# Kernel optimization log

Hardware: AMD Instinct MI355X
Metric: run time of the kernel (lower is better)

## Reference

```python
import jax, jax.numpy as jnp
import numpy as np

KS = 3
PAD = 1
STRIDE = 1


def _conv2d(x, w, b=None, stride=1, padding=0):
    out = jax.lax.conv_general_dilated(
        x, w, (stride, stride), [(padding, padding), (padding, padding)],
        dimension_numbers=("NCHW", "OIHW", "NCHW"))
    if b is not None:
        out = out + b[None, :, None, None]
    return out


def _p_n(N):
    # torch.meshgrid(a, a, indexing='xy') -> X[i,j]=a[j], Y[i,j]=a[i]
    a = np.arange(-(KS - 1) // 2, (KS - 1) // 2 + 1)
    X, Y = np.meshgrid(a, a, indexing="xy")
    p_n = np.concatenate([X.flatten(), Y.flatten()], 0).astype(np.float32)
    return jnp.asarray(p_n.reshape(1, 2 * N, 1, 1))


def _p_0(h, w, N):
    av = np.arange(1, h * STRIDE + 1, STRIDE)
    bv = np.arange(1, w * STRIDE + 1, STRIDE)
    X, Y = np.meshgrid(av, bv, indexing="xy")  # shape (w, h), replicates torch quirk
    p0x = np.tile(X.flatten().reshape(1, 1, h, w), (1, N, 1, 1))
    p0y = np.tile(Y.flatten().reshape(1, 1, h, w), (1, N, 1, 1))
    return jnp.asarray(np.concatenate([p0x, p0y], 1).astype(np.float32))


def setup_inputs() -> dict:
    key = jax.random.key(0)
    k1, k2, k3, k4 = jax.random.split(key, 4)
    B, C, H, W = 2, 64, 256, 256
    x = jax.random.normal(k1, (B, C, H, W), dtype=jnp.float32)
    p_conv_w = jax.random.normal(k2, (2 * KS * KS, C, 3, 3), dtype=jnp.float32) * 0.01
    p_conv_b = jax.random.normal(k3, (2 * KS * KS,), dtype=jnp.float32) * 0.1
    conv_w = jax.random.normal(k4, (64, C, KS, KS), dtype=jnp.float32) * 0.05
    return {"x": x, "p_conv_w": p_conv_w, "p_conv_b": p_conv_b, "conv_w": conv_w}


def _deform_conv(x, p_conv_w, p_conv_b, conv_w):
    B, C = x.shape[0], x.shape[1]
    offset = _conv2d(x, p_conv_w, p_conv_b, stride=STRIDE, padding=1)  # (B, 2N, h, w)
    N = offset.shape[1] // 2
    h, w = offset.shape[2], offset.shape[3]
    xp = jnp.pad(x, ((0, 0), (0, 0), (PAD, PAD), (PAD, PAD)))
    Hp, Wp = xp.shape[2], xp.shape[3]

    p = _p_0(h, w, N) + _p_n(N) + offset            # (B, 2N, h, w)
    p = p.transpose(0, 2, 3, 1)                      # (B, h, w, 2N)

    def clampxy(t):
        return jnp.concatenate(
            [jnp.clip(t[..., :N], 0, Hp - 1), jnp.clip(t[..., N:], 0, Wp - 1)], -1)

    q_lt = clampxy(jnp.floor(jax.lax.stop_gradient(p)))
    q_rb = clampxy(jnp.floor(jax.lax.stop_gradient(p)) + 1)
    q_lt = q_lt.astype(jnp.int32)
    q_rb = q_rb.astype(jnp.int32)
    q_lb = jnp.concatenate([q_lt[..., :N], q_rb[..., N:]], -1)
    q_rt = jnp.concatenate([q_rb[..., :N], q_lt[..., N:]], -1)

    p = clampxy(p)
    px, py = p[..., :N], p[..., N:]

    def bilin_w(q):
        qx = q[..., :N].astype(p.dtype)
        qy = q[..., N:].astype(p.dtype)
        return qx - px, qy - py

    dx_lt, dy_lt = bilin_w(q_lt)
    dx_rb, dy_rb = bilin_w(q_rb)
    g_lt = (1 + dx_lt) * (1 + dy_lt)
    g_rb = (1 - dx_rb) * (1 - dy_rb)
    g_lb = (1 + dx_lt) * (1 - dy_rb)   # q_lb = (lt_x, rb_y)
    g_rt = (1 - dx_rb) * (1 + dy_lt)   # q_rt = (rb_x, lt_y)

    xf = xp.reshape(B, C, Hp * Wp)

    def gather(q):
        idx = q[..., :N] * Wp + q[..., N:]                     # (B, h, w, N)
        idxb = jnp.broadcast_to(idx.reshape(B, 1, -1), (B, C, h * w * N))
        return jnp.take_along_axis(xf, idxb, axis=2).reshape(B, C, h, w, N)

    x_off = (g_lt[:, None] * gather(q_lt) + g_rb[:, None] * gather(q_rb)
             + g_lb[:, None] * gather(q_lb) + g_rt[:, None] * gather(q_rt))

    # 'b c h w (kh kw) -> b c (h kh) (w kw)'
    x_off = x_off.reshape(B, C, h, w, KS, KS).transpose(0, 1, 2, 4, 3, 5)
    x_off = x_off.reshape(B, C, h * KS, w * KS)
    return _conv2d(x_off, conv_w, stride=KS)


def reference(x, p_conv_w, p_conv_b, conv_w):
    return _deform_conv(x, p_conv_w, p_conv_b, conv_w)
```

## Files before the change

### kernel.cpp

```cpp
#include <hip/hip_runtime.h>

#define HW   256
#define HW2  (HW * HW)
#define CIN  64
#define COUT 64

#define RXN   7
#define CYN   70
#define NSITE (RXN * CYN)
#define SSTR  48

#define ONS   198
#define OSTR  144

typedef __attribute__((ext_vector_type(8))) short short8v;
typedef __attribute__((ext_vector_type(4))) float f32x4;
typedef __attribute__((ext_vector_type(4))) unsigned uint4v;

__device__ __forceinline__ unsigned short f2bf(float f) {
  unsigned u = __float_as_uint(f);
  u = u + 0x7FFFu + ((u >> 16) & 1u);
  return (unsigned short)(u >> 16);
}
__device__ __forceinline__ unsigned cvt_pk_bf16(float lo, float hi) {
  unsigned r;
  asm("v_cvt_pk_bf16_f32 %0, %1, %2" : "=v"(r) : "v"(lo), "v"(hi));
  return r;
}

__global__ void wfrag_kernel(const float* __restrict__ w, const float* __restrict__ pw,
                             short* __restrict__ wf, short* __restrict__ wf2) {
  const int T = blockIdx.x * 256 + threadIdx.x;
  if (T < 5120) {
    const int l    = T & 63;
    const int t    = (T >> 6) & 3;
    const int g    = T >> 8;
    const int j    = g % 5;
    const int rho  = g / 5;
    const int half = (l >> 5) & 1;
    const int oct  = (l >> 4) & 1;
    const int n    = 2 * j + half;
    const int oc   = t * 16 + (l & 15);
    const int ic0  = rho * 16 + oct * 8;
    short8v v;
#pragma unroll
    for (int e = 0; e < 8; ++e)
      v[e] = (n < 9) ? (short)f2bf(w[(oc * CIN + ic0 + e) * 9 + n]) : (short)0;
    *(short8v*)(wf + (size_t)T * 8) = v;
  } else if (T < 7680) {
    const int T2   = T - 5120;
    const int l    = T2 & 63;
    const int t    = (T2 >> 6) & 1;
    const int g    = T2 >> 7;
    const int j    = g % 5;
    const int rho  = g / 5;
    const int half = (l >> 5) & 1;
    const int oct  = (l >> 4) & 1;
    const int n    = 2 * j + half;
    const int oc   = t * 16 + (l & 15);
    const int ic0  = rho * 16 + oct * 8;
    short8v v;
#pragma unroll
    for (int e = 0; e < 8; ++e)
      v[e] = (n < 9 && oc < 18) ? (short)f2bf(pw[(oc * CIN + ic0 + e) * 9 + n])
                                : (short)0;
    *(short8v*)(wf2 + (size_t)T2 * 8) = v;
  }
}

__global__ __launch_bounds__(256) void offs_mfma_kernel(
    const float* __restrict__ x, const short* __restrict__ wf2,
    const float* __restrict__ pb, float* __restrict__ off)
{
  __shared__ __align__(16) char sow[ONS * OSTR];

  const int b    = blockIdx.y;
  const int bx   = blockIdx.x;
  const int r0   = (bx & 3) * 64;
  const int c0   = bx >> 2;
  const int tid  = threadIdx.x;
  const int lane = tid & 63;
  const int i    = lane & 15;
  const int g4   = lane >> 4;
  const int oct  = g4 & 1;
  const int half = g4 >> 1;
  const int wv   = tid >> 6;
  const int r    = r0 + wv * 16 + i;

  if (tid < ONS) {
    const int rl = tid / 3, kw = tid - rl * 3;
    const int rr = r0 - 1 + rl;
    const int cc = c0 - 1 + kw;
    const bool ok = (rr >= 0) & (rr < HW) & (cc >= 0) & (cc < HW);
    const float* xq = x + (size_t)b * CIN * HW2
                    + (size_t)max(rr, 0) * HW + max(cc, 0);
    char* dst = sow + tid * OSTR;
#pragma unroll
    for (int m8 = 0; m8 < 8; ++m8) {
      uint4v v;
#pragma unroll
      for (int mm = 0; mm < 4; ++mm) {
        const int pl = m8 * 8 + mm * 2;
        const float v0 = ok ? xq[(size_t)pl * HW2] : 0.f;
        const float v1 = ok ? xq[(size_t)(pl + 1) * HW2] : 0.f;
        v[mm] = cvt_pk_bf16(v0, v1);
      }
      *(uint4v*)(dst + m8 * 16) = v;
    }
  }
  __syncthreads();

  f32x4 acc0 = (f32x4){0.f, 0.f, 0.f, 0.f};
  f32x4 acc1 = (f32x4){0.f, 0.f, 0.f, 0.f};

#pragma unroll
  for (int rho = 0; rho < 4; ++rho) {
#pragma unroll
    for (int j = 0; j < 5; ++j) {
      const int n  = 2 * j + half;
      const int nn = (n < 9) ? n : 0;
      const int kh = nn / 3, kw = nn - kh * 3;
      const int site = (wv * 16 + i + kh) * 3 + kw;
      const short8v bfr = *(const short8v*)(sow + site * OSTR + rho * 32 + oct * 16);
      const short* wfb = wf2 + ((size_t)(((rho * 5 + j) * 2) * 64) + lane) * 8;
      const short8v a0 = *(const short8v*)(wfb);
      const short8v a1 = *(const short8v*)(wfb + 64 * 8);
      acc0 = __builtin_amdgcn_mfma_f32_16x16x32_bf16(a0, bfr, acc0, 0, 0, 0);
      acc1 = __builtin_amdgcn_mfma_f32_16x16x32_bf16(a1, bfr, acc1, 0, 0, 0);
    }
  }

  float* ob = off + (size_t)(b * HW + c0) * 18 * HW;
#pragma unroll
  for (int jj = 0; jj < 4; ++jj) {
    const int ch = g4 * 4 + jj;
    ob[(size_t)ch * HW + r] = acc0[jj] + pb[ch];
  }
  if (g4 == 0) {
#pragma unroll
    for (int jj = 0; jj < 2; ++jj) {
      const int ch = 16 + jj;
      ob[(size_t)ch * HW + r] = acc1[jj] + pb[ch];
    }
  }
}

__global__ __launch_bounds__(256)
__attribute__((amdgpu_waves_per_eu(2, 4)))
void deform_kernel(
    const float* __restrict__ x, const float* __restrict__ off,
    const short* __restrict__ wf, float* __restrict__ out)
{
  __shared__ __align__(16) char sxb[NSITE * SSTR];

  const int b    = blockIdx.y;
  const int bx   = blockIdx.x;
  const int r0   = (bx & 3) * 64;
  const int c0   = bx >> 2;
  const int tid  = threadIdx.x;
  const int lane = tid & 63;
  const int i    = lane & 15;
  const int a    = (lane >> 4) & 3;
  const int oct  = a & 1;
  const int half = a >> 1;
  const int wv   = tid >> 6;
  const int r    = r0 + wv * 16 + i;

  unsigned qsite[5];
  float    qwx[5], qwy[5];
  unsigned inwm = 0;
  const float* obp = off + (size_t)(b * HW + c0) * 18 * HW;
#pragma unroll
  for (int t5 = 0; t5 < 5; ++t5) {
    const int  n9  = 2 * t5 + half;
    const bool pad = (n9 >= 9);
    const int  n   = pad ? 0 : n9;
    const float ox = obp[(size_t)n * HW + r];
    const float oy = obp[(size_t)(9 + n) * HW + r];
    const float px = (float)(c0 + (n % 3)) + ox;
    const float py = (float)(r + (n / 3)) + oy;
    const float fx = floorf(px);
    const float fy = floorf(py);
    const int ltx = (int)fx, lty = (int)fy;
    const bool okc = (ltx >= 0) & (lty >= 0) & (ltx + 1 <= HW + 1) & (lty + 1 <= HW + 1);
    const int lx = ltx - c0 + 2;
    const int ly = lty - r0 + 2;
    const bool inw = okc & (lx >= 0) & (lx <= RXN - 2) & (ly >= 0) & (ly <= CYN - 2);
    qsite[t5] = (pad || !inw) ? 0u : (unsigned)(lx * CYN + ly);
    qwx[t5]   = 1.f + fx - px;
    qwy[t5]   = 1.f + fy - py;
    inwm |= ((inw || pad) ? 1u : 0u) << t5;
  }

  const int s1 = tid, s2 = tid + 256;
  int gi1 = 0, gi2 = 0; bool ok1, ok2;
  {
    const int rxl = s1 / CYN, cyl = s1 - rxl * CYN;
    const int rx = c0 - 2 + rxl, cyp = r0 - 2 + cyl;
    ok1 = (rx >= 1) & (rx <= HW) & (cyp >= 1) & (cyp <= HW);
    if (ok1) gi1 = (rx - 1) * HW + (cyp - 1);
  }
  {
    const int rxl = s2 / CYN, cyl = s2 - rxl * CYN;
    const int rx = c0 - 2 + rxl, cyp = r0 - 2 + cyl;
    ok2 = (s2 < NSITE) & (rx >= 1) & (rx <= HW) & (cyp >= 1) & (cyp <= HW);
    if (ok2) gi2 = (rx - 1) * HW + (cyp - 1);
  }

  const float* xb = x + (size_t)b * CIN * HW2;

  float pv1[16], pv2[16];

#define LOADR(RHO)                                                         \
  {                                                                        \
    const float* xsrc = xb + (size_t)((RHO) * 16) * HW2;                   \
    _Pragma("unroll")                                                      \
    for (int m = 0; m < 16; ++m) {                                         \
      const float* xp = xsrc + (size_t)m * HW2;                            \
      pv1[m] = ok1 ? xp[gi1] : 0.f;                                        \
      pv2[m] = ok2 ? xp[gi2] : 0.f;                                        \
    }                                                                      \
  }

#define WRITES()                                                           \
  {                                                                        \
    uint4v w0, w1;                                                         \
    _Pragma("unroll")                                                      \
    for (int m = 0; m < 4; ++m) w0[m] = cvt_pk_bf16(pv1[2*m], pv1[2*m+1]); \
    _Pragma("unroll")                                                      \
    for (int m = 0; m < 4; ++m) w1[m] = cvt_pk_bf16(pv1[8+2*m], pv1[9+2*m]);\
    *(uint4v*)(sxb + s1 * SSTR)      = w0;                                 \
    *(uint4v*)(sxb + s1 * SSTR + 16) = w1;                                 \
    if (s2 < NSITE) {                                                      \
      uint4v u0, u1;                                                       \
      _Pragma("unroll")                                                    \
      for (int m = 0; m < 4; ++m) u0[m] = cvt_pk_bf16(pv2[2*m], pv2[2*m+1]);\
      _Pragma("unroll")                                                    \
      for (int m = 0; m < 4; ++m) u1[m] = cvt_pk_bf16(pv2[8+2*m], pv2[9+2*m]);\
      *(uint4v*)(sxb + s2 * SSTR)      = u0;                               \
      *(uint4v*)(sxb + s2 * SSTR + 16) = u1;                               \
    }                                                                      \
  }

  f32x4 acc[4];
#pragma unroll
  for (int t = 0; t < 4; ++t) acc[t] = (f32x4){0.f, 0.f, 0.f, 0.f};

  LOADR(0)
  WRITES()
  __syncthreads();

#pragma unroll 1
  for (int rho = 0; rho < 4; ++rho) {
    if (rho < 3) LOADR(rho + 1)

    const short* wfr = wf + ((size_t)(rho * 5 * 4) * 64 + lane) * 8;
    const char*  sbo = sxb + oct * 16;

    uint4v nA, nB, nC, nD;
    {
      const char* pb_ = sbo + qsite[0] * SSTR;
      nA = *(const uint4v*)(pb_);
      nC = *(const uint4v*)(pb_ + SSTR);
      nD = *(const uint4v*)(pb_ + 70 * SSTR);
      nB = *(const uint4v*)(pb_ + 71 * SSTR);
    }

#define TAPBODY(J)                                                          \
    {                                                                       \
       \
      const short* wfb_ = wfr + (size_t)(J) * 4 * 64 * 8;                   \
      const short8v af0 = *(const short8v*)(wfb_);                          \
      const short8v af1 = *(const short8v*)(wfb_ + 1 * 64 * 8);             \
      const short8v af2 = *(const short8v*)(wfb_ + 2 * 64 * 8);             \
      const short8v af3 = *(const short8v*)(wfb_ + 3 * 64 * 8);             \
      const uint4v A = nA, B = nB, C = nC, D = nD;                          \
      if ((J) < 4) {                       \
        const char* pb_ = sbo + qsite[(J) + 1] * SSTR;                      \
        nA = *(const uint4v*)(pb_);                                         \
        nC = *(const uint4v*)(pb_ + SSTR);                                  \
        nD = *(const uint4v*)(pb_ + 70 * SSTR);                             \
        nB = *(const uint4v*)(pb_ + 71 * SSTR);                             \
      }                                                                     \
      short8v bfr;                                                          \
      if (__all((inwm >> (J)) & 1)) {                                       \
        const float wxl = qwx[J], wyl = qwy[J];                             \
        const float wxr = 1.f - wxl, wyr = 1.f - wyl;                       \
        const float g0 = wxl * wyl, g1 = wxr * wyr;                         \
        const float g2 = wxl * wyr, g3 = wxr * wyl;                         \
        uint4v bw;                                                          \
        _Pragma("unroll")                                                   \
        for (int m = 0; m < 4; ++m) {                                       \
          const float alo = __uint_as_float(A[m] << 16);                    \
          const float ahi = __uint_as_float(A[m] & 0xFFFF0000u);            \
          const float blo = __uint_as_float(B[m] << 16);                    \
          const float bhi = __uint_as_float(B[m] & 0xFFFF0000u);            \
          const float clo = __uint_as_float(C[m] << 16);                    \
          const float chi = __uint_as_float(C[m] & 0xFFFF0000u);            \
          const float dlo = __uint_as_float(D[m] << 16);                    \
          const float dhi = __uint_as_float(D[m] & 0xFFFF0000u);            \
          float sl = g0 * alo;                                              \
          sl = fmaf(g1, blo, sl); sl = fmaf(g2, clo, sl);                   \
          sl = fmaf(g3, dlo, sl);                                           \
          float sh = g0 * ahi;                                              \
          sh = fmaf(g1, bhi, sh); sh = fmaf(g2, chi, sh);                   \
          sh = fmaf(g3, dhi, sh);                                           \
          bw[m] = cvt_pk_bf16(sl, sh);                                      \
        }                                                                   \
        bfr = __builtin_bit_cast(short8v, bw);                              \
      } else {                                                              \
         \
        const int  n9_  = 2 * (J) + half;                                   \
        const bool pad_ = (n9_ >= 9);                                       \
        const int  n_   = pad_ ? 0 : n9_;                                   \
        const float ox_ = obp[(size_t)n_ * HW + r];                         \
        const float oy_ = obp[(size_t)(9 + n_) * HW + r];                   \
        const float px_ = (float)(c0 + (n_ % 3)) + ox_;                     \
        const float py_ = (float)(r + (n_ / 3)) + oy_;                      \
        const float fx_ = floorf(px_);                                      \
        const float fy_ = floorf(py_);                                      \
        int ltx_ = (int)fx_, lty_ = (int)fy_;                               \
        int rbx_ = ltx_ + 1, rby_ = lty_ + 1;                               \
        ltx_ = min(max(ltx_, 0), HW + 1); lty_ = min(max(lty_, 0), HW + 1); \
        rbx_ = min(max(rbx_, 0), HW + 1); rby_ = min(max(rby_, 0), HW + 1); \
        const float pxc_ = fminf(fmaxf(px_, 0.f), (float)(HW + 1));         \
        const float pyc_ = fminf(fmaxf(py_, 0.f), (float)(HW + 1));         \
        const float wxl_ = 1.f + (float)ltx_ - pxc_;                        \
        const float wxr_ = 1.f - ((float)rbx_ - pxc_);                      \
        const float wyl_ = 1.f + (float)lty_ - pyc_;                        \
        const float wyr_ = 1.f - ((float)rby_ - pyc_);                      \
        const int   cxs_[4] = { ltx_, rbx_, ltx_, rbx_ };                   \
        const int   cys_[4] = { lty_, rby_, rby_, lty_ };                   \
        const float cgs_[4] = { wxl_ * wyl_, wxr_ * wyr_,                   \
                                wxl_ * wyr_, wxr_ * wyl_ };                 \
        int gi_[4]; float gw_[4];                                           \
        _Pragma("unroll")                                                   \
        for (int k = 0; k < 4; ++k) {                                       \
          const bool ok_ = (cxs_[k] >= 1) & (cxs_[k] <= HW) &               \
                           (cys_[k] >= 1) & (cys_[k] <= HW);                \
          gi_[k] = ok_ ? ((cxs_[k] - 1) * HW + (cys_[k] - 1)) : 0;          \
          gw_[k] = (ok_ && !pad_) ? cgs_[k] : 0.f;                          \
        }                                                                   \
        const float* xpl_ = xb + (size_t)(rho * 16 + oct * 8) * HW2;        \
        _Pragma("unroll")                                                   \
        for (int e = 0; e < 8; ++e) {                                       \
          const float* xe_ = xpl_ + (size_t)e * HW2;                        \
          float sv_ = gw_[0] * xe_[gi_[0]];                                 \
          sv_ = fmaf(gw_[1], xe_[gi_[1]], sv_);                             \
          sv_ = fmaf(gw_[2], xe_[gi_[2]], sv_);                             \
          sv_ = fmaf(gw_[3], xe_[gi_[3]], sv_);                             \
          bfr[e] = (short)f2bf(sv_);                                        \
        }                                                                   \
      }                                                                     \
      acc[0] = __builtin_amdgcn_mfma_f32_16x16x32_bf16(af0, bfr, acc[0], 0, 0, 0); \
      acc[1] = __builtin_amdgcn_mfma_f32_16x16x32_bf16(af1, bfr, acc[1], 0, 0, 0); \
      acc[2] = __builtin_amdgcn_mfma_f32_16x16x32_bf16(af2, bfr, acc[2], 0, 0, 0); \
      acc[3] = __builtin_amdgcn_mfma_f32_16x16x32_bf16(af3, bfr, acc[3], 0, 0, 0); \
    }

    TAPBODY(0) TAPBODY(1) TAPBODY(2) TAPBODY(3) TAPBODY(4)
#undef TAPBODY

    __syncthreads();
    if (rho < 3) {
      WRITES()
      __syncthreads();
    }
  }

#pragma unroll
  for (int t = 0; t < 4; ++t)
#pragma unroll
    for (int jj = 0; jj < 4; ++jj) {
      const int oc = t * 16 + a * 4 + jj;
      out[((size_t)(b * COUT + oc)) * HW2 + (size_t)r * HW + c0] = acc[t][jj];
    }
#undef LOADR
#undef WRITES
}

extern "C" void kernel_launch(void* const* d_in, const int* in_sizes, int n_in,
                              void* d_out, int out_size, void* d_ws, size_t ws_size,
                              hipStream_t stream) {
  const float* x  = (const float*)d_in[0];
  const float* pw = (const float*)d_in[1];
  const float* pb = (const float*)d_in[2];
  const float* w  = (const float*)d_in[3];
  float* out = (float*)d_out;

  char* wsb = (char*)d_ws;
  float* off = (float*)wsb;
  short* wfg = (short*)(wsb + (size_t)2 * 18 * HW2 * 4);
  short* wf2 = (short*)(wsb + (size_t)2 * 18 * HW2 * 4 + 81920);

  wfrag_kernel<<<30, 256, 0, stream>>>(w, pw, wfg, wf2);
  dim3 grid(1024, 2);
  offs_mfma_kernel<<<grid, 256, 0, stream>>>(x, wf2, pb, off);
  deform_kernel<<<grid, 256, 0, stream>>>(x, off, wfg, out);
}
```

Measured before the change: 164.3 us.

## Fuse offset-conv MFMA kernel into deform kernel via shared-memory offsets

Merges the offset convolution kernel into the deformable sampling kernel. Each block first computes its 18 offset channels for its 64-pixel column tile with MFMA and stores them in LDS, then runs the deform gather and conv reading offsets from LDS instead of a global buffer. This removes the global round-trip of the offset tensor and one kernel launch. In exchange LDS use per block grows, which may reduce occupancy, and the offset stage's x staging is serialized ahead of the deform work in the same block.

```diff
diff --git a/kernel.cpp b/kernel.cpp
--- a/kernel.cpp
+++ b/kernel.cpp
@@ -13,8 +13,10 @@
 #define ONS   198
 #define OSTR  144
 
-typedef __attribute__((ext_vector_type(8))) short short8v;
-typedef __attribute__((ext_vector_type(4))) float f32x4;
+#define SOFF_BYTES 4608
+
+typedef __attribute__((ext_vector_type(8))) short    short8v;
+typedef __attribute__((ext_vector_type(4))) float    f32x4;
 typedef __attribute__((ext_vector_type(4))) unsigned uint4v;
 
 __device__ __forceinline__ unsigned short f2bf(float f) {
@@ -68,90 +70,17 @@
   }
 }
 
-__global__ __launch_bounds__(256) void offs_mfma_kernel(
-    const float* __restrict__ x, const short* __restrict__ wf2,
-    const float* __restrict__ pb, float* __restrict__ off)
-{
-  __shared__ __align__(16) char sow[ONS * OSTR];
-
-  const int b    = blockIdx.y;
-  const int bx   = blockIdx.x;
-  const int r0   = (bx & 3) * 64;
-  const int c0   = bx >> 2;
-  const int tid  = threadIdx.x;
-  const int lane = tid & 63;
-  const int i    = lane & 15;
-  const int g4   = lane >> 4;
-  const int oct  = g4 & 1;
-  const int half = g4 >> 1;
-  const int wv   = tid >> 6;
-  const int r    = r0 + wv * 16 + i;
-
-  if (tid < ONS) {
-    const int rl = tid / 3, kw = tid - rl * 3;
-    const int rr = r0 - 1 + rl;
-    const int cc = c0 - 1 + kw;
-    const bool ok = (rr >= 0) & (rr < HW) & (cc >= 0) & (cc < HW);
-    const float* xq = x + (size_t)b * CIN * HW2
-                    + (size_t)max(rr, 0) * HW + max(cc, 0);
-    char* dst = sow + tid * OSTR;
-#pragma unroll
-    for (int m8 = 0; m8 < 8; ++m8) {
-      uint4v v;
-#pragma unroll
-      for (int mm = 0; mm < 4; ++mm) {
-        const int pl = m8 * 8 + mm * 2;
-        const float v0 = ok ? xq[(size_t)pl * HW2] : 0.f;
-        const float v1 = ok ? xq[(size_t)(pl + 1) * HW2] : 0.f;
-        v[mm] = cvt_pk_bf16(v0, v1);
-      }
-      *(uint4v*)(dst + m8 * 16) = v;
-    }
-  }
-  __syncthreads();
-
-  f32x4 acc0 = (f32x4){0.f, 0.f, 0.f, 0.f};
-  f32x4 acc1 = (f32x4){0.f, 0.f, 0.f, 0.f};
-
-#pragma unroll
-  for (int rho = 0; rho < 4; ++rho) {
-#pragma unroll
-    for (int j = 0; j < 5; ++j) {
-      const int n  = 2 * j + half;
-      const int nn = (n < 9) ? n : 0;
-      const int kh = nn / 3, kw = nn - kh * 3;
-      const int site = (wv * 16 + i + kh) * 3 + kw;
-      const short8v bfr = *(const short8v*)(sow + site * OSTR + rho * 32 + oct * 16);
-      const short* wfb = wf2 + ((size_t)(((rho * 5 + j) * 2) * 64) + lane) * 8;
-      const short8v a0 = *(const short8v*)(wfb);
-      const short8v a1 = *(const short8v*)(wfb + 64 * 8);
-      acc0 = __builtin_amdgcn_mfma_f32_16x16x32_bf16(a0, bfr, acc0, 0, 0, 0);
-      acc1 = __builtin_amdgcn_mfma_f32_16x16x32_bf16(a1, bfr, acc1, 0, 0, 0);
-    }
-  }
-
-  float* ob = off + (size_t)(b * HW + c0) * 18 * HW;
-#pragma unroll
-  for (int jj = 0; jj < 4; ++jj) {
-    const int ch = g4 * 4 + jj;
-    ob[(size_t)ch * HW + r] = acc0[jj] + pb[ch];
-  }
-  if (g4 == 0) {
-#pragma unroll
-    for (int jj = 0; jj < 2; ++jj) {
-      const int ch = 16 + jj;
-      ob[(size_t)ch * HW + r] = acc1[jj] + pb[ch];
-    }
-  }
-}
-
 __global__ __launch_bounds__(256)
 __attribute__((amdgpu_waves_per_eu(2, 4)))
-void deform_kernel(
-    const float* __restrict__ x, const float* __restrict__ off,
-    const short* __restrict__ wf, float* __restrict__ out)
+void fused_kernel(
+    const float* __restrict__ x, const short* __restrict__ wf,
+    const short* __restrict__ wf2, const float* __restrict__ pb,
+    float* __restrict__ out)
 {
-  __shared__ __align__(16) char sxb[NSITE * SSTR];
+  __shared__ __align__(16) char smem[SOFF_BYTES + ONS * OSTR];
+  float* sOffT = (float*)smem;
+  char*  sow   = smem + SOFF_BYTES;
+  char*  sxb   = smem + SOFF_BYTES;
 
   const int b    = blockIdx.y;
   const int bx   = blockIdx.x;
@@ -164,19 +93,77 @@
   const int oct  = a & 1;
   const int half = a >> 1;
   const int wv   = tid >> 6;
-  const int r    = r0 + wv * 16 + i;
+  const int rr   = wv * 16 + i;
+  const int r    = r0 + rr;
+
+  const float* xb = x + (size_t)b * CIN * HW2;
+
+  if (tid < ONS) {
+    const int rl = tid / 3, kw = tid - rl * 3;
+    const int rw = r0 - 1 + rl;
+    const int cc = c0 - 1 + kw;
+    const bool ok = (rw >= 0) & (rw < HW) & (cc >= 0) & (cc < HW);
+    const float* xq = xb + (size_t)max(rw, 0) * HW + max(cc, 0);
+    char* dst = sow + tid * OSTR;
+#pragma unroll
+    for (int m8 = 0; m8 < 8; ++m8) {
+      uint4v v;
+#pragma unroll
+      for (int mm = 0; mm < 4; ++mm) {
+        const int pl = m8 * 8 + mm * 2;
+        const float v0 = ok ? xq[(size_t)pl * HW2] : 0.f;
+        const float v1 = ok ? xq[(size_t)(pl + 1) * HW2] : 0.f;
+        v[mm] = cvt_pk_bf16(v0, v1);
+      }
+      *(uint4v*)(dst + m8 * 16) = v;
+    }
+  }
+  __syncthreads();
+
+  {
+    f32x4 acc0 = (f32x4){0.f, 0.f, 0.f, 0.f};
+    f32x4 acc1 = (f32x4){0.f, 0.f, 0.f, 0.f};
+#pragma unroll
+    for (int rho = 0; rho < 4; ++rho) {
+#pragma unroll
+      for (int j = 0; j < 5; ++j) {
+        const int n  = 2 * j + half;
+        const int nn = (n < 9) ? n : 0;
+        const int kh = nn / 3, kw = nn - kh * 3;
+        const int site = (rr + kh) * 3 + kw;
+        const short8v bfr = *(const short8v*)(sow + site * OSTR + rho * 32 + oct * 16);
+        const short* wfb = wf2 + ((size_t)(((rho * 5 + j) * 2) * 64) + lane) * 8;
+        const short8v a0 = *(const short8v*)(wfb);
+        const short8v a1 = *(const short8v*)(wfb + 64 * 8);
+        acc0 = __builtin_amdgcn_mfma_f32_16x16x32_bf16(a0, bfr, acc0, 0, 0, 0);
+        acc1 = __builtin_amdgcn_mfma_f32_16x16x32_bf16(a1, bfr, acc1, 0, 0, 0);
+      }
+    }
+#pragma unroll
+    for (int jj = 0; jj < 4; ++jj) {
+      const int ch = a * 4 + jj;
+      sOffT[ch * 64 + rr] = acc0[jj] + pb[ch];
+    }
+    if (a == 0) {
+#pragma unroll
+      for (int jj = 0; jj < 2; ++jj) {
+        const int ch = 16 + jj;
+        sOffT[ch * 64 + rr] = acc1[jj] + pb[ch];
+      }
+    }
+  }
+  __syncthreads();
 
   unsigned qsite[5];
   float    qwx[5], qwy[5];
   unsigned inwm = 0;
-  const float* obp = off + (size_t)(b * HW + c0) * 18 * HW;
 #pragma unroll
   for (int t5 = 0; t5 < 5; ++t5) {
     const int  n9  = 2 * t5 + half;
     const bool pad = (n9 >= 9);
     const int  n   = pad ? 0 : n9;
-    const float ox = obp[(size_t)n * HW + r];
-    const float oy = obp[(size_t)(9 + n) * HW + r];
+    const float ox = sOffT[n * 64 + rr];
+    const float oy = sOffT[(9 + n) * 64 + rr];
     const float px = (float)(c0 + (n % 3)) + ox;
     const float py = (float)(r + (n / 3)) + oy;
     const float fx = floorf(px);
@@ -206,8 +193,6 @@
     ok2 = (s2 < NSITE) & (rx >= 1) & (rx <= HW) & (cyp >= 1) & (cyp <= HW);
     if (ok2) gi2 = (rx - 1) * HW + (cyp - 1);
   }
-
-  const float* xb = x + (size_t)b * CIN * HW2;
 
   float pv1[16], pv2[16];
 
@@ -275,8 +260,8 @@
       const short8v af2 = *(const short8v*)(wfb_ + 2 * 64 * 8);             \
       const short8v af3 = *(const short8v*)(wfb_ + 3 * 64 * 8);             \
       const uint4v A = nA, B = nB, C = nC, D = nD;                          \
-      if ((J) < 4) {                       \
-        const char* pb_ = sbo + qsite[(J) + 1] * SSTR;                      \
+      if ((J) < 4) {               \
+        const char* pb_ = sbo + qsite[(J) < 4 ? (J) + 1 : 0] * SSTR;        \
         nA = *(const uint4v*)(pb_);                                         \
         nC = *(const uint4v*)(pb_ + SSTR);                                  \
         nD = *(const uint4v*)(pb_ + 70 * SSTR);                             \
@@ -313,8 +298,8 @@
         const int  n9_  = 2 * (J) + half;                                   \
         const bool pad_ = (n9_ >= 9);                                       \
         const int  n_   = pad_ ? 0 : n9_;                                   \
-        const float ox_ = obp[(size_t)n_ * HW + r];                         \
-        const float oy_ = obp[(size_t)(9 + n_) * HW + r];                   \
+        const float ox_ = sOffT[n_ * 64 + rr];                              \
+        const float oy_ = sOffT[(9 + n_) * 64 + rr];                        \
         const float px_ = (float)(c0 + (n_ % 3)) + ox_;                     \
         const float py_ = (float)(r + (n_ / 3)) + oy_;                      \
         const float fx_ = floorf(px_);                                      \
@@ -389,12 +374,10 @@
   float* out = (float*)d_out;
 
   char* wsb = (char*)d_ws;
-  float* off = (float*)wsb;
-  short* wfg = (short*)(wsb + (size_t)2 * 18 * HW2 * 4);
-  short* wf2 = (short*)(wsb + (size_t)2 * 18 * HW2 * 4 + 81920);
+  short* wfg = (short*)wsb;
+  short* wf2 = (short*)(wsb + 81920);
 
   wfrag_kernel<<<30, 256, 0, stream>>>(w, pw, wfg, wf2);
   dim3 grid(1024, 2);
-  offs_mfma_kernel<<<grid, 256, 0, stream>>>(x, wf2, pb, off);
-  deform_kernel<<<grid, 256, 0, stream>>>(x, off, wfg, out);
-}
+  fused_kernel<<<grid, 256, 0, stream>>>(x, wfg, wf2, pb, out);
+}
```

New measurement: 174.0 us. 1.06x slower.
